# Optimization experiments

Measured on AMD Instinct MI355X. Metric: run time of the kernel, lower is better.

The kernel has to match this reference:

```python
import jax, jax.numpy as jnp
import numpy as np

B, L, D = 8192, 2048, 256


def setup_inputs() -> dict:
    key = jax.random.key(0)
    kx, kl = jax.random.split(key)
    x = jax.random.normal(kx, (B, D), dtype=jnp.float32)
    landmarks = jax.random.normal(kl, (L, D), dtype=jnp.float32)
    return {"x": x, "landmarks": landmarks}


def reference(x, landmarks):
    # RBF layer: out[b, l] = exp(-gamma * sum_d (landmarks[l, d] - x[b, d])^2)
    # gamma='auto' -> 1 / n_features (landmarks.shape[1])
    gamma = jnp.float32(1.0 / landmarks.shape[1])
    # avoids materializing the [B, L, D] broadcast-diff intermediate)
    x2 = jnp.sum(x * x, axis=-1, keepdims=True)          # [B, 1]
    l2 = jnp.sum(landmarks * landmarks, axis=-1)         # [L]
    cross = jnp.einsum('bd,ld->bl', x, landmarks)        # [B, L]
    d2 = jnp.maximum(x2 + l2[None, :] - 2.0 * cross, 0.0)
    return jnp.exp(-gamma * d2)
```

## Files before the change

### kernel.cpp

```cpp
#include <hip/hip_runtime.h>


typedef __bf16 bf16x8 __attribute__((ext_vector_type(8)));
typedef float  f32x4  __attribute__((ext_vector_type(4)));

#define B_ROWS 8192
#define L_ROWS 2048
#define K_DIM  256

#define GLD_LDS(g, l) __builtin_amdgcn_global_load_lds(                      \
    (const __attribute__((address_space(1))) void*)(g),                      \
    (__attribute__((address_space(3))) void*)(l), 16, 0, 0)

__device__ __forceinline__ unsigned short f32_to_bf16_rne(float f) {
    union { float f; unsigned int u; } v; v.f = f;
    unsigned int u = v.u;
    unsigned int r = (u + 0x7fffu + ((u >> 16) & 1u)) >> 16;
    return (unsigned short)r;
}

__global__ __launch_bounds__(256) void cvt_rows_kernel(
    const float* __restrict__ x, const float* __restrict__ lm,
    unsigned short* __restrict__ xb, unsigned short* __restrict__ lb,
    float* __restrict__ x2, float* __restrict__ l2)
{
    const int lane = threadIdx.x & 63;
    const int gw   = blockIdx.x * 4 + (threadIdx.x >> 6);
    const float* in; unsigned short* outb; float* sq; int row;
    if (gw < B_ROWS) { in = x;  outb = xb; sq = x2; row = gw; }
    else             { in = lm; outb = lb; sq = l2; row = gw - B_ROWS; }
    const float4 v = ((const float4*)(in + (size_t)row * K_DIM))[lane];
    ushort4 o;
    o.x = f32_to_bf16_rne(v.x);
    o.y = f32_to_bf16_rne(v.y);
    o.z = f32_to_bf16_rne(v.z);
    o.w = f32_to_bf16_rne(v.w);
    ((ushort4*)(outb + (size_t)row * K_DIM))[lane] = o;
    float s = v.x*v.x + v.y*v.y + v.z*v.z + v.w*v.w;
    #pragma unroll
    for (int off = 32; off > 0; off >>= 1) s += __shfl_down(s, off, 64);
    if (lane == 0) sq[row] = s;
}

__global__ __launch_bounds__(256) void rbf_gemm_kernel(
    const unsigned short* __restrict__ A,
    const unsigned short* __restrict__ Bm,
    const float* __restrict__ x2,
    const float* __restrict__ l2,
    float* __restrict__ out)
{
    __shared__ unsigned short As[2][128 * 64];
    __shared__ unsigned short Bs[2][128 * 64];

    const int tid  = threadIdx.x;
    const int wave = tid >> 6;
    const int lane = tid & 63;
    const int wm = wave >> 1, wn = wave & 1;
    const int bm = blockIdx.x, bn = blockIdx.y;

    f32x4 acc[4][4];
    #pragma unroll
    for (int i = 0; i < 4; ++i)
        #pragma unroll
        for (int j = 0; j < 4; ++j)
            acc[i][j] = (f32x4){0.f, 0.f, 0.f, 0.f};

    const int ldrow = lane >> 3;
    const int ldcol = (((lane & 7) ^ ldrow) * 8);

    const unsigned short* Ab = A  + (size_t)(bm * 128) * K_DIM;
    const unsigned short* Bb = Bm + (size_t)(bn * 128) * K_DIM;

#define STAGE(buf, k0)                                                       \
    _Pragma("unroll")                                                        \
    for (int it = 0; it < 4; ++it) {                                         \
        const int r = wave * 32 + it * 8;                                    \
        GLD_LDS(Ab + (r + ldrow) * K_DIM + (k0) + ldcol, &As[buf][r * 64]);  \
        GLD_LDS(Bb + (r + ldrow) * K_DIM + (k0) + ldcol, &Bs[buf][r * 64]);  \
    }

    STAGE(0, 0);

    const int xr = (lane & 7) << 4;

    #pragma unroll
    for (int t = 0; t < 4; ++t) {
        const int cur = t & 1;
        if (t < 3) { STAGE(cur ^ 1, (t + 1) * 64); }
        if (t < 3) asm volatile("s_waitcnt vmcnt(8)" ::: "memory");
        else       asm volatile("s_waitcnt vmcnt(0)" ::: "memory");
        asm volatile("s_barrier" ::: "memory");

        #pragma unroll
        for (int kk = 0; kk < 64; kk += 32) {
            const int osw = ((kk * 2 + (lane >> 4) * 16) ^ xr) >> 1;
            bf16x8 af[4], bfr[4];
            #pragma unroll
            for (int tt = 0; tt < 4; ++tt) {
                af[tt]  = *(const bf16x8*)&As[cur][(wm*64 + tt*16 + (lane & 15)) * 64 + osw];
                bfr[tt] = *(const bf16x8*)&Bs[cur][(wn*64 + tt*16 + (lane & 15)) * 64 + osw];
            }
            #pragma unroll
            for (int mt = 0; mt < 4; ++mt)
                #pragma unroll
                for (int nt = 0; nt < 4; ++nt)
                    acc[mt][nt] = __builtin_amdgcn_mfma_f32_16x16x32_bf16(
                        bfr[nt], af[mt], acc[mt][nt], 0, 0, 0);
        }
        if (t < 3) asm volatile("s_barrier" ::: "memory");
    }
#undef STAGE

    const float gamma = 1.0f / 256.0f;
    const int row0 = bm * 128 + wm * 64 + (lane & 15);
    const int col0 = bn * 128 + wn * 64 + (lane >> 4) * 4;

    float xv[4];
    #pragma unroll
    for (int mt = 0; mt < 4; ++mt) xv[mt] = x2[row0 + mt * 16];
    f32x4 lv[4];
    #pragma unroll
    for (int nt = 0; nt < 4; ++nt) lv[nt] = *(const f32x4*)&l2[col0 + nt * 16];

    #pragma unroll
    for (int mt = 0; mt < 4; ++mt) {
        const size_t rb = (size_t)(row0 + mt * 16) * L_ROWS;
        #pragma unroll
        for (int nt = 0; nt < 4; ++nt) {
            f32x4 v;
            #pragma unroll
            for (int r = 0; r < 4; ++r) {
                float d2 = fmaxf(xv[mt] + lv[nt][r] - 2.0f * acc[mt][nt][r], 0.0f);
                v[r] = __expf(-gamma * d2);
            }
            *((f32x4*)&out[rb + col0 + nt * 16]) = v;
        }
    }
}

extern "C" void kernel_launch(void* const* d_in, const int* in_sizes, int n_in,
                              void* d_out, int out_size, void* d_ws, size_t ws_size,
                              hipStream_t stream) {
    const float* x  = (const float*)d_in[0];
    const float* lm = (const float*)d_in[1];
    float* out = (float*)d_out;

    char* ws = (char*)d_ws;
    unsigned short* xb = (unsigned short*)ws;
    unsigned short* lb = (unsigned short*)(ws + (size_t)B_ROWS*K_DIM*2);
    float* x2 = (float*)(ws + (size_t)B_ROWS*K_DIM*2 + (size_t)L_ROWS*K_DIM*2);
    float* l2 = x2 + B_ROWS;

    cvt_rows_kernel<<<(B_ROWS + L_ROWS)/4, 256, 0, stream>>>(x, lm, xb, lb, x2, l2);
    rbf_gemm_kernel<<<dim3(B_ROWS/128, L_ROWS/128), 256, 0, stream>>>(xb, lb, x2, l2, out);
}
```

Measured before the change: 91.88 us.

## Enlarge GEMM tile to 256x256 with 8 waves, XCD-aware block mapping, nontemporal stores

The RBF GEMM block tile grows from 128x128 to 256x256 using 512 threads, each wave computing a 128x64 sub-tile. This cuts redundant global and LDS loads of the bf16 operands. The grid becomes a 256-block 1D launch, with a block-id remap that spreads neighbouring tiles across XCDs. Output stores become nontemporal so the large fp32 result does not pollute the cache. In exchange, LDS use doubles to about 128KB and the accumulators double, which limits each CU to a single block and raises register pressure.

Result: slower. 98.31 us (+7.0%).

```diff
diff --git a/kernel.cpp b/kernel.cpp
--- a/kernel.cpp
+++ b/kernel.cpp
@@ -42,25 +42,30 @@
     if (lane == 0) sq[row] = s;
 }
 
-__global__ __launch_bounds__(256) void rbf_gemm_kernel(
+__global__ __launch_bounds__(512, 2) void rbf_gemm_kernel(
     const unsigned short* __restrict__ A,
     const unsigned short* __restrict__ Bm,
     const float* __restrict__ x2,
     const float* __restrict__ l2,
     float* __restrict__ out)
 {
-    __shared__ unsigned short As[2][128 * 64];
-    __shared__ unsigned short Bs[2][128 * 64];
+    __shared__ unsigned short As[2][256 * 64];
+    __shared__ unsigned short Bs[2][256 * 64];
 
     const int tid  = threadIdx.x;
     const int wave = tid >> 6;
     const int lane = tid & 63;
-    const int wm = wave >> 1, wn = wave & 1;
-    const int bm = blockIdx.x, bn = blockIdx.y;
+    const int wm = wave >> 2;
+    const int wn = wave & 3;
 
-    f32x4 acc[4][4];
+    const int bid = blockIdx.x;
+    const int wg  = (bid & 7) * 32 + (bid >> 3);
+    const int bm  = wg & 31;
+    const int bn  = wg >> 5;
+
+    f32x4 acc[8][4];
     #pragma unroll
-    for (int i = 0; i < 4; ++i)
+    for (int i = 0; i < 8; ++i)
         #pragma unroll
         for (int j = 0; j < 4; ++j)
             acc[i][j] = (f32x4){0.f, 0.f, 0.f, 0.f};
@@ -68,8 +73,8 @@
     const int ldrow = lane >> 3;
     const int ldcol = (((lane & 7) ^ ldrow) * 8);
 
-    const unsigned short* Ab = A  + (size_t)(bm * 128) * K_DIM;
-    const unsigned short* Bb = Bm + (size_t)(bn * 128) * K_DIM;
+    const unsigned short* Ab = A  + (size_t)(bm * 256) * K_DIM;
+    const unsigned short* Bb = Bm + (size_t)(bn * 256) * K_DIM;
 
 #define STAGE(buf, k0)                                                       \
     _Pragma("unroll")                                                        \
@@ -94,14 +99,15 @@
         #pragma unroll
         for (int kk = 0; kk < 64; kk += 32) {
             const int osw = ((kk * 2 + (lane >> 4) * 16) ^ xr) >> 1;
-            bf16x8 af[4], bfr[4];
+            bf16x8 af[8], bfr[4];
             #pragma unroll
-            for (int tt = 0; tt < 4; ++tt) {
-                af[tt]  = *(const bf16x8*)&As[cur][(wm*64 + tt*16 + (lane & 15)) * 64 + osw];
-                bfr[tt] = *(const bf16x8*)&Bs[cur][(wn*64 + tt*16 + (lane & 15)) * 64 + osw];
-            }
+            for (int nt = 0; nt < 4; ++nt)
+                bfr[nt] = *(const bf16x8*)&Bs[cur][(wn*64 + nt*16 + (lane & 15)) * 64 + osw];
             #pragma unroll
-            for (int mt = 0; mt < 4; ++mt)
+            for (int mt = 0; mt < 8; ++mt)
+                af[mt]  = *(const bf16x8*)&As[cur][(wm*128 + mt*16 + (lane & 15)) * 64 + osw];
+            #pragma unroll
+            for (int mt = 0; mt < 8; ++mt)
                 #pragma unroll
                 for (int nt = 0; nt < 4; ++nt)
                     acc[mt][nt] = __builtin_amdgcn_mfma_f32_16x16x32_bf16(
@@ -112,28 +118,27 @@
 #undef STAGE
 
     const float gamma = 1.0f / 256.0f;
-    const int row0 = bm * 128 + wm * 64 + (lane & 15);
-    const int col0 = bn * 128 + wn * 64 + (lane >> 4) * 4;
+    const int row0 = bm * 256 + wm * 128 + (lane & 15);
+    const int col0 = bn * 256 + wn * 64 + (lane >> 4) * 4;
 
-    float xv[4];
-    #pragma unroll
-    for (int mt = 0; mt < 4; ++mt) xv[mt] = x2[row0 + mt * 16];
     f32x4 lv[4];
     #pragma unroll
     for (int nt = 0; nt < 4; ++nt) lv[nt] = *(const f32x4*)&l2[col0 + nt * 16];
 
     #pragma unroll
-    for (int mt = 0; mt < 4; ++mt) {
-        const size_t rb = (size_t)(row0 + mt * 16) * L_ROWS;
+    for (int mt = 0; mt < 8; ++mt) {
+        const int row = row0 + mt * 16;
+        const float xv = x2[row];
+        const size_t rb = (size_t)row * L_ROWS;
         #pragma unroll
         for (int nt = 0; nt < 4; ++nt) {
             f32x4 v;
             #pragma unroll
             for (int r = 0; r < 4; ++r) {
-                float d2 = fmaxf(xv[mt] + lv[nt][r] - 2.0f * acc[mt][nt][r], 0.0f);
+                float d2 = fmaxf(xv + lv[nt][r] - 2.0f * acc[mt][nt][r], 0.0f);
                 v[r] = __expf(-gamma * d2);
             }
-            *((f32x4*)&out[rb + col0 + nt * 16]) = v;
+            __builtin_nontemporal_store(v, (f32x4*)&out[rb + col0 + nt * 16]);
         }
     }
 }
@@ -152,5 +157,5 @@
     float* l2 = x2 + B_ROWS;
 
     cvt_rows_kernel<<<(B_ROWS + L_ROWS)/4, 256, 0, stream>>>(x, lm, xb, lb, x2, l2);
-    rbf_gemm_kernel<<<dim3(B_ROWS/128, L_ROWS/128), 256, 0, stream>>>(xb, lb, x2, l2, out);
+    rbf_gemm_kernel<<<256, 512, 0, stream>>>(xb, lb, x2, l2, out);
 }
```

## Load A fragments directly to registers, remap blocks per XCD, use nontemporal stores

Applied to the files above, without the earlier changes.

The A tile is no longer staged through LDS. Each wave now loads its MFMA A fragments straight from global memory into registers, which halves LDS use and traffic and changes the wait counts. The launch becomes a 1D grid with an XCD-aware remap, so blocks sharing the same A rows run on one XCD and can reuse L2. Output stores become nontemporal to avoid polluting the cache with the 64MB result. The risks are uncoalesced direct global loads for A and that loads duplicated across the two wn waves now go through L1/L2 instead of being shared in LDS.

Result: slower. 111.0 us (+20.8%).

```diff
diff --git a/kernel.cpp b/kernel.cpp
--- a/kernel.cpp
+++ b/kernel.cpp
@@ -49,14 +49,18 @@
     const float* __restrict__ l2,
     float* __restrict__ out)
 {
-    __shared__ unsigned short As[2][128 * 64];
     __shared__ unsigned short Bs[2][128 * 64];
 
     const int tid  = threadIdx.x;
     const int wave = tid >> 6;
     const int lane = tid & 63;
     const int wm = wave >> 1, wn = wave & 1;
-    const int bm = blockIdx.x, bn = blockIdx.y;
+
+    const int bid = blockIdx.x;
+    const int xcd = bid & 7;
+    const int idx = bid >> 3;
+    const int bm  = xcd * 8 + (idx & 7);
+    const int bn  = idx >> 3;
 
     f32x4 acc[4][4];
     #pragma unroll
@@ -68,72 +72,77 @@
     const int ldrow = lane >> 3;
     const int ldcol = (((lane & 7) ^ ldrow) * 8);
 
-    const unsigned short* Ab = A  + (size_t)(bm * 128) * K_DIM;
     const unsigned short* Bb = Bm + (size_t)(bn * 128) * K_DIM;
+    const unsigned short* Ap = A + (size_t)(bm * 128 + wm * 64 + (lane & 15)) * K_DIM
+                                 + (lane >> 4) * 8;
 
-#define STAGE(buf, k0)                                                       \
+#define STAGE_B(buf, k0)                                                     \
     _Pragma("unroll")                                                        \
     for (int it = 0; it < 4; ++it) {                                         \
         const int r = wave * 32 + it * 8;                                    \
-        GLD_LDS(Ab + (r + ldrow) * K_DIM + (k0) + ldcol, &As[buf][r * 64]);  \
         GLD_LDS(Bb + (r + ldrow) * K_DIM + (k0) + ldcol, &Bs[buf][r * 64]);  \
     }
 
-    STAGE(0, 0);
+    STAGE_B(0, 0);
 
     const int xr = (lane & 7) << 4;
 
     #pragma unroll
     for (int t = 0; t < 4; ++t) {
         const int cur = t & 1;
-        if (t < 3) { STAGE(cur ^ 1, (t + 1) * 64); }
-        if (t < 3) asm volatile("s_waitcnt vmcnt(8)" ::: "memory");
+        const int k0 = t * 64;
+
+        bf16x8 af[4][2];
+        #pragma unroll
+        for (int mt = 0; mt < 4; ++mt) {
+            af[mt][0] = *(const bf16x8*)&Ap[(size_t)mt * 16 * K_DIM + k0];
+            af[mt][1] = *(const bf16x8*)&Ap[(size_t)mt * 16 * K_DIM + k0 + 32];
+        }
+        if (t < 3) { STAGE_B(cur ^ 1, k0 + 64); }
+        if (t < 3) asm volatile("s_waitcnt vmcnt(4)" ::: "memory");
         else       asm volatile("s_waitcnt vmcnt(0)" ::: "memory");
         asm volatile("s_barrier" ::: "memory");
 
         #pragma unroll
         for (int kk = 0; kk < 64; kk += 32) {
             const int osw = ((kk * 2 + (lane >> 4) * 16) ^ xr) >> 1;
-            bf16x8 af[4], bfr[4];
+            bf16x8 bfr[4];
             #pragma unroll
-            for (int tt = 0; tt < 4; ++tt) {
-                af[tt]  = *(const bf16x8*)&As[cur][(wm*64 + tt*16 + (lane & 15)) * 64 + osw];
-                bfr[tt] = *(const bf16x8*)&Bs[cur][(wn*64 + tt*16 + (lane & 15)) * 64 + osw];
-            }
+            for (int nt = 0; nt < 4; ++nt)
+                bfr[nt] = *(const bf16x8*)&Bs[cur][(wn*64 + nt*16 + (lane & 15)) * 64 + osw];
             #pragma unroll
             for (int mt = 0; mt < 4; ++mt)
                 #pragma unroll
                 for (int nt = 0; nt < 4; ++nt)
                     acc[mt][nt] = __builtin_amdgcn_mfma_f32_16x16x32_bf16(
-                        bfr[nt], af[mt], acc[mt][nt], 0, 0, 0);
+                        bfr[nt], af[mt][kk >> 5], acc[mt][nt], 0, 0, 0);
         }
         if (t < 3) asm volatile("s_barrier" ::: "memory");
     }
-#undef STAGE
+#undef STAGE_B
 
     const float gamma = 1.0f / 256.0f;
     const int row0 = bm * 128 + wm * 64 + (lane & 15);
     const int col0 = bn * 128 + wn * 64 + (lane >> 4) * 4;
 
-    float xv[4];
-    #pragma unroll
-    for (int mt = 0; mt < 4; ++mt) xv[mt] = x2[row0 + mt * 16];
     f32x4 lv[4];
     #pragma unroll
     for (int nt = 0; nt < 4; ++nt) lv[nt] = *(const f32x4*)&l2[col0 + nt * 16];
 
     #pragma unroll
     for (int mt = 0; mt < 4; ++mt) {
-        const size_t rb = (size_t)(row0 + mt * 16) * L_ROWS;
+        const int row = row0 + mt * 16;
+        const float xv = x2[row];
+        const size_t rb = (size_t)row * L_ROWS;
         #pragma unroll
         for (int nt = 0; nt < 4; ++nt) {
             f32x4 v;
             #pragma unroll
             for (int r = 0; r < 4; ++r) {
-                float d2 = fmaxf(xv[mt] + lv[nt][r] - 2.0f * acc[mt][nt][r], 0.0f);
+                float d2 = fmaxf(xv + lv[nt][r] - 2.0f * acc[mt][nt][r], 0.0f);
                 v[r] = __expf(-gamma * d2);
             }
-            *((f32x4*)&out[rb + col0 + nt * 16]) = v;
+            __builtin_nontemporal_store(v, (f32x4*)&out[rb + col0 + nt * 16]);
         }
     }
 }
@@ -152,5 +161,5 @@
     float* l2 = x2 + B_ROWS;
 
     cvt_rows_kernel<<<(B_ROWS + L_ROWS)/4, 256, 0, stream>>>(x, lm, xb, lb, x2, l2);
-    rbf_gemm_kernel<<<dim3(B_ROWS/128, L_ROWS/128), 256, 0, stream>>>(xb, lb, x2, l2, out);
+    rbf_gemm_kernel<<<1024, 256, 0, stream>>>(xb, lb, x2, l2, out);
 }
```
